# Optimization experiments

Hardware: AMD Instinct MI355X
Metric: run time of the kernel (lower is better)

Reference implementation:

```python
import jax, jax.numpy as jnp
import numpy as np
from jax import lax

F_DIM = 128
H_DIM = 128
K_NN = 16
S_PTS = 512
EPS = 1e-5


def _layernorm(x, g, b):
    m = jnp.mean(x, -1, keepdims=True)
    v = jnp.mean((x - m) ** 2, -1, keepdims=True)
    return (x - m) * lax.rsqrt(v + EPS) * g + b


def _batchnorm(x, g, b):
    # training-mode BN over (batch, points, neighbors) per channel; x: [B,S,K,C]
    m = jnp.mean(x, (0, 1, 2))
    v = jnp.mean((x - m) ** 2, (0, 1, 2))
    return (x - m) * lax.rsqrt(v + EPS) * g + b


def _gather(x, idx):
    # x: [B,R,C], idx: [B,...] int -> [B,...,C]
    return jax.vmap(lambda a, i: a[i])(x, idx)


def _fps(xyz, S):
    # farthest point sampling, deterministic start at index 0 (pytorch3d default)
    B, N, _ = xyz.shape
    idx0 = jnp.zeros((B,), jnp.int32)

    def step(carry, _):
        mind, last = carry
        p = jax.vmap(lambda a, i: a[i])(xyz, last)  # [B,3]
        d = jnp.sum((xyz - p[:, None]) ** 2, -1)  # [B,N]
        mind = jnp.minimum(mind, d)
        nxt = jnp.argmax(mind, -1).astype(jnp.int32)
        return (mind, nxt), nxt

    init = (jnp.full((B, N), 1e10, xyz.dtype), idx0)
    _, rest = lax.scan(step, init, None, length=S - 1)
    return jnp.concatenate([idx0[None], rest], 0).T  # [B,S]


def _knn_idx(q, ref, K):
    # squared dists [B,Q,R]; top-K nearest, sorted ascending by distance
    d2 = (jnp.sum(q * q, -1)[:, :, None] + jnp.sum(ref * ref, -1)[:, None, :]
          - 2.0 * jnp.einsum('bqd,brd->bqr', q, ref))
    _, idx = lax.top_k(-d2, K)
    return idx


def setup_inputs() -> dict:
    key = jax.random.key(0)
    ks = jax.random.split(key, 32)
    B, N, F, H = 4, 8192, F_DIM, H_DIM
    w = lambda k, shp: (jax.random.normal(k, shp, jnp.float32) * 0.02)
    return {
        'xyzp': jax.random.uniform(ks[0], (B, N, 4), jnp.float32),
        'features': jax.random.normal(ks[1], (B, N, F), jnp.float32),
        'ln_g': jnp.ones((F,), jnp.float32), 'ln_b': jnp.zeros((F,), jnp.float32),
        'td_w0': w(ks[2], (F + 3, F)), 'td_b0': jnp.zeros((F,), jnp.float32),
        'td_bn0_g': jnp.ones((F,), jnp.float32), 'td_bn0_b': jnp.zeros((F,), jnp.float32),
        'td_w1': w(ks[3], (F, F)), 'td_b1': jnp.zeros((F,), jnp.float32),
        'td_bn1_g': jnp.ones((F,), jnp.float32), 'td_bn1_b': jnp.zeros((F,), jnp.float32),
        'w_kern': w(ks[4], (F, H)), 'b_kern': jnp.zeros((H,), jnp.float32),
        'w_gkern': w(ks[5], (F, H)), 'b_gkern': jnp.zeros((H,), jnp.float32),
        'w_agg': w(ks[6], (H, F)), 'b_agg': jnp.zeros((F,), jnp.float32),
        'w_q': w(ks[7], (H, H)), 'w_k': w(ks[8], (H, H)), 'w_v': w(ks[9], (H, H)),
        'pe_w1': w(ks[10], (4, H)), 'pe_b1': jnp.zeros((H,), jnp.float32),
        'pe_w2': w(ks[11], (H, H)), 'pe_b2': jnp.zeros((H,), jnp.float32),
        'at_w1': w(ks[12], (H, H)), 'at_b1': jnp.zeros((H,), jnp.float32),
        'at_w2': w(ks[13], (H, H)), 'at_b2': jnp.zeros((H,), jnp.float32),
    }


def reference(xyzp, features, ln_g, ln_b, td_w0, td_b0, td_bn0_g, td_bn0_b,
              td_w1, td_b1, td_bn1_g, td_bn1_b, w_kern, b_kern, w_gkern, b_gkern,
              w_agg, b_agg, w_q, w_k, w_v, pe_w1, pe_b1, pe_w2, pe_b2,
              at_w1, at_b1, at_w2, at_b2):
    feats = _layernorm(features, ln_g, ln_b)
    xyz = xyzp[:, :, :3]
    # ---- TransitionDown ----
    fps_idx = _fps(xyz, S_PTS)                       # [B,S]
    new_xyz = _gather(xyz, fps_idx)                  # [B,S,3]
    idx_dn = _knn_idx(new_xyz, xyz, K_NN)            # [B,S,K]
    new_xyzp = _gather(xyzp, idx_dn)[:, :, 0]        # [B,S,4] nearest = self
    grouped_xyz = _gather(xyz, idx_dn) - new_xyz[:, :, None]   # [B,S,K,3]
    grouped_feat = _gather(feats, idx_dn)            # [B,S,K,F]
    h = jnp.concatenate([grouped_xyz, grouped_feat], -1)
    h = jax.nn.relu(_batchnorm(h @ td_w0 + td_b0, td_bn0_g, td_bn0_b))
    h = jax.nn.relu(_batchnorm(h @ td_w1 + td_b1, td_bn1_g, td_bn1_b))
    new_feats = jnp.max(h, axis=2)                   # [B,S,F]
    # ---- vector attention over K global neighbors ----
    idx_up = _knn_idx(xyz, new_xyz, K_NN)            # [B,N,K]
    pdiff = xyzp[:, :, None] - _gather(new_xyzp, idx_up)  # [B,N,K,4]
    pos_enc = jax.nn.relu(pdiff @ pe_w1 + pe_b1) @ pe_w2 + pe_b2
    x = feats @ w_kern + b_kern                      # [B,N,H]
    new_x = new_feats @ w_gkern + b_gkern            # [B,S,H]
    q = x @ w_q
    k = _gather(new_x @ w_k, idx_up)                 # [B,N,K,H]
    v = _gather(new_x @ w_v, idx_up)
    a = q[:, :, None] - k + pos_enc
    a = jax.nn.relu(a @ at_w1 + at_b1) @ at_w2 + at_b2
    a = jax.nn.softmax(a / np.float32(np.sqrt(H_DIM)), axis=2)  # softmax over neighbors
    res = jnp.sum(a * (v + pos_enc), axis=2)         # einsum bmnf,bmnf->bmf
    return res @ w_agg + b_agg + feats
```

## Files before the change

### kernel.cpp

```cpp
#include <hip/hip_runtime.h>

constexpr int B = 4, N = 8192, S = 512, K = 16, F = 128, H = 128;
constexpr float EPS = 1e-5f;

typedef short v8s __attribute__((ext_vector_type(8)));
typedef float v4f __attribute__((ext_vector_type(4)));

__device__ __forceinline__ short f2bf(float x) {
  union { float f; unsigned u; } v; v.f = x;
  unsigned r = v.u + 0x7fffu + ((v.u >> 16) & 1u);
  return (short)(r >> 16);
}
__device__ __forceinline__ float bf2f(short s) {
  union { unsigned u; float f; } v; v.u = ((unsigned)(unsigned short)s) << 16;
  return v.f;
}

template <int CTRL>
__device__ __forceinline__ float dpp_mov_f(float v) {
  return __int_as_float(__builtin_amdgcn_update_dpp(
      __float_as_int(v), __float_as_int(v), CTRL, 0xF, 0xF, false));
}
template <int CTRL>
__device__ __forceinline__ int dpp_mov_i(int v) {
  return __builtin_amdgcn_update_dpp(v, v, CTRL, 0xF, 0xF, false);
}

__global__ __launch_bounds__(256) void wconv_kernel(
    const float* __restrict__ pe_w2, const float* __restrict__ at_w1,
    const float* __restrict__ at_w2, const float* __restrict__ w_kern,
    const float* __restrict__ w_q, const float* __restrict__ td_w1,
    const float* __restrict__ td_w0, short* __restrict__ wbf) {
  int i = blockIdx.x * 256 + threadIdx.x;
  if (i < 6 * 16384) {
    int m = i >> 14, e = i & 16383;
    const float* src = m == 0 ? pe_w2 : m == 1 ? at_w1 : m == 2 ? at_w2
                     : m == 3 ? w_kern : m == 4 ? w_q : td_w1;
    int kx = e >> 7, n = e & 127;
    wbf[m * 16384 + n * 128 + kx] = f2bf(src[e]);
  } else {
    int e = i - 6 * 16384;
    int n = e / 160, kz = e % 160;
    short v = (kz < 131) ? f2bf(td_w0[kz * 128 + n]) : (short)0;
    wbf[6 * 16384 + n * 160 + kz] = v;
  }
}

__global__ __launch_bounds__(256) void ln_kernel(const float* __restrict__ features,
    const float* __restrict__ g, const float* __restrict__ bta, float* __restrict__ feats) {
  int r = blockIdx.x * 4 + (threadIdx.x >> 6);
  int lane = threadIdx.x & 63;
  const float2* fp = (const float2*)(features + (size_t)r * F);
  float2 v = fp[lane];
  float s = v.x + v.y;
  #pragma unroll
  for (int off = 32; off > 0; off >>= 1) s += __shfl_xor(s, off);
  float m = s * (1.f / F);
  float dx = v.x - m, dy = v.y - m;
  float s2 = dx * dx + dy * dy;
  #pragma unroll
  for (int off = 32; off > 0; off >>= 1) s2 += __shfl_xor(s2, off);
  float rstd = rsqrtf(s2 * (1.f / F) + EPS);
  float2 gg = ((const float2*)g)[lane];
  float2 bb = ((const float2*)bta)[lane];
  float2* op = (float2*)(feats + (size_t)r * F);
  op[lane] = make_float2(dx * rstd * gg.x + bb.x, dy * rstd * gg.y + bb.y);
}

__global__ __launch_bounds__(256, 1) void fps_kernel(const float* __restrict__ xyzp,
    float* __restrict__ new_xyz) {
  __shared__ float4 xl4[N];
  __shared__ float nx[S * 3];
  __shared__ float2 slot[2][4];
  int b = blockIdx.x, t = threadIdx.x;
  int lane = t & 63, wid = t >> 6;
  const float4* xp = (const float4*)(xyzp + (size_t)b * N * 4);
  float px[32], py[32], pz[32], mind[32];
  #pragma unroll
  for (int j = 0; j < 32; j++) {
    int idx = t + 256 * j;
    float4 p = xp[idx];
    px[j] = p.x; py[j] = p.y; pz[j] = p.z; mind[j] = 1e10f;
    xl4[idx] = p;
  }
  __syncthreads();
  float4 p0 = xl4[0];
  float cx = p0.x, cy = p0.y, cz = p0.z;
  if (t == 0) { nx[0] = cx; nx[1] = cy; nx[2] = cz; }
  for (int s = 1; s < S; ++s) {
    float bv = -1.f; int bj = 0;
    #pragma unroll
    for (int j = 0; j < 32; j++) {
      float dx = __fsub_rn(px[j], cx), dy = __fsub_rn(py[j], cy), dz = __fsub_rn(pz[j], cz);
      float d = __fadd_rn(__fadd_rn(__fmul_rn(dx, dx), __fmul_rn(dy, dy)), __fmul_rn(dz, dz));
      mind[j] = fminf(mind[j], d);
      if (mind[j] > bv) { bv = mind[j]; bj = j; }
    }
    int bi = t + (bj << 8);
    #define FPS_STEP(CTRL) { \
      float ov = dpp_mov_f<CTRL>(bv); int oi = dpp_mov_i<CTRL>(bi); \
      if (ov > bv || (ov == bv && oi < bi)) { bv = ov; bi = oi; } }
    FPS_STEP(0x111) FPS_STEP(0x112) FPS_STEP(0x114) FPS_STEP(0x118)
    FPS_STEP(0x142) FPS_STEP(0x143)
    #undef FPS_STEP
    int par = s & 1;
    if (lane == 63) slot[par][wid] = make_float2(bv, __int_as_float(bi));
    __syncthreads();
    float2 s0 = slot[par][0], s1 = slot[par][1], s2 = slot[par][2], s3 = slot[par][3];
    int i0 = __float_as_int(s0.y), i1 = __float_as_int(s1.y);
    int i2 = __float_as_int(s2.y), i3 = __float_as_int(s3.y);
    float4 c0v = xl4[i0], c1v = xl4[i1], c2v = xl4[i2], c3v = xl4[i3];
    float v0 = s0.x, v1 = s1.x, v2 = s2.x, v3 = s3.x;
    bool m01 = (v1 > v0) || (v1 == v0 && i1 < i0);
    float va = m01 ? v1 : v0; int ia = m01 ? i1 : i0;
    bool m23 = (v3 > v2) || (v3 == v2 && i3 < i2);
    float vb = m23 ? v3 : v2; int ib = m23 ? i3 : i2;
    bool mf = (vb > va) || (vb == va && ib < ia);
    float cax = m01 ? c1v.x : c0v.x, cay = m01 ? c1v.y : c0v.y, caz = m01 ? c1v.z : c0v.z;
    float cbx = m23 ? c3v.x : c2v.x, cby = m23 ? c3v.y : c2v.y, cbz = m23 ? c3v.z : c2v.z;
    cx = mf ? cbx : cax; cy = mf ? cby : cay; cz = mf ? cbz : caz;
    if (t == 0) { nx[s * 3 + 0] = cx; nx[s * 3 + 1] = cy; nx[s * 3 + 2] = cz; }
  }
  __syncthreads();
  for (int i = t; i < S * 3; i += 256)
    new_xyz[(size_t)b * S * 3 + i] = nx[i];
}

__global__ __launch_bounds__(256) void knn_dn_kernel(const float* __restrict__ xyzp,
    const float* __restrict__ new_xyz, int* __restrict__ idx_dn, float* __restrict__ new_xyzp) {
  int wave = threadIdx.x >> 6, lane = threadIdx.x & 63;
  int qid = blockIdx.x * 4 + wave;
  int b = qid >> 9, s = qid & (S - 1);
  const float4* xp = (const float4*)(xyzp + (size_t)b * N * 4);
  float qx = new_xyz[((size_t)b * S + s) * 3 + 0];
  float qy = new_xyz[((size_t)b * S + s) * 3 + 1];
  float qz = new_xyz[((size_t)b * S + s) * 3 + 2];
  float qq = __fadd_rn(__fadd_rn(__fmul_rn(qx, qx), __fmul_rn(qy, qy)), __fmul_rn(qz, qz));

  float lastD = -1.f; int lastI = -1;
  float D1, D2; int I1, I2;
  auto scan2 = [&]() {
    D1 = 3e38f; I1 = 0x7fffffff; D2 = 3e38f; I2 = 0x7fffffff;
    for (int j = 0; j < 128; j++) {
      int i = lane + 64 * j;
      float4 p = xp[i];
      float rr  = __fadd_rn(__fadd_rn(__fmul_rn(p.x, p.x), __fmul_rn(p.y, p.y)), __fmul_rn(p.z, p.z));
      float dot = __fadd_rn(__fadd_rn(__fmul_rn(qx, p.x), __fmul_rn(qy, p.y)), __fmul_rn(qz, p.z));
      float d2 = __fsub_rn(__fadd_rn(qq, rr), __fmul_rn(2.0f, dot));
      bool gate = (d2 > lastD) || (d2 == lastD && i > lastI);
      bool b1   = (d2 < D1) || (d2 == D1 && i < I1);
      bool b2   = (d2 < D2) || (d2 == D2 && i < I2);
      if (gate && b1)      { D2 = D1; I2 = I1; D1 = d2; I1 = i; }
      else if (gate && b2) { D2 = d2; I2 = i; }
    }
  };
  scan2();
  int outI = 0;
  float4 nn0;
  #pragma unroll 1
  for (int r = 0; r < K; r++) {
    float mD = D1; int mI = I1; int mL = lane;
    #pragma unroll
    for (int off = 32; off > 0; off >>= 1) {
      float od = __shfl_xor(mD, off); int oi = __shfl_xor(mI, off); int ol = __shfl_xor(mL, off);
      if (od < mD || (od == mD && oi < mI)) { mD = od; mI = oi; mL = ol; }
    }
    if (lane == r) outI = mI;
    if (r == 0 && lane == 0) nn0 = xp[mI];
    if (lane == mL) {
      lastD = mD; lastI = mI;
      if (I2 != 0x7fffffff) { D1 = D2; I1 = I2; D2 = 3e38f; I2 = 0x7fffffff; }
      else scan2();
    }
  }
  size_t base = ((size_t)b * S + s) * K;
  if (lane < K) idx_dn[base + lane] = outI;
  if (lane == 0) *(float4*)&new_xyzp[((size_t)b * S + s) * 4] = nn0;
}

__global__ __launch_bounds__(256) void knn_up_kernel(const float* __restrict__ xyzp,
    const float* __restrict__ new_xyz, int* __restrict__ idx_up) {
  int wave = threadIdx.x >> 6, lane = threadIdx.x & 63;
  int qid = blockIdx.x * 4 + wave;
  int b = qid >> 13, n = qid & (N - 1);
  const float4* xp = (const float4*)(xyzp + (size_t)b * N * 4);
  float4 qp = xp[n];
  float qx = qp.x, qy = qp.y, qz = qp.z;
  float qq = __fadd_rn(__fadd_rn(__fmul_rn(qx, qx), __fmul_rn(qy, qy)), __fmul_rn(qz, qz));
  float rx[8], ry[8], rz[8];
  #pragma unroll
  for (int j = 0; j < 8; j++) {
    int i = lane + 64 * j;
    rx[j] = new_xyz[((size_t)b * S + i) * 3 + 0];
    ry[j] = new_xyz[((size_t)b * S + i) * 3 + 1];
    rz[j] = new_xyz[((size_t)b * S + i) * 3 + 2];
  }
  float lastD = -1.f; int lastI = -1;
  float D1, D2; int I1, I2;
  auto scan2 = [&]() {
    D1 = 3e38f; I1 = 0x7fffffff; D2 = 3e38f; I2 = 0x7fffffff;
    #pragma unroll
    for (int j = 0; j < 8; j++) {
      int i = lane + 64 * j;
      float rr  = __fadd_rn(__fadd_rn(__fmul_rn(rx[j], rx[j]), __fmul_rn(ry[j], ry[j])), __fmul_rn(rz[j], rz[j]));
      float dot = __fadd_rn(__fadd_rn(__fmul_rn(qx, rx[j]), __fmul_rn(qy, ry[j])), __fmul_rn(qz, rz[j]));
      float d2 = __fsub_rn(__fadd_rn(qq, rr), __fmul_rn(2.0f, dot));
      bool gate = (d2 > lastD) || (d2 == lastD && i > lastI);
      bool b1   = (d2 < D1) || (d2 == D1 && i < I1);
      bool b2   = (d2 < D2) || (d2 == D2 && i < I2);
      if (gate && b1)      { D2 = D1; I2 = I1; D1 = d2; I1 = i; }
      else if (gate && b2) { D2 = d2; I2 = i; }
    }
  };
  scan2();
  int outI = 0;
  #pragma unroll 1
  for (int r = 0; r < K; r++) {
    float mD = D1; int mI = I1; int mL = lane;
    #pragma unroll
    for (int off = 32; off > 0; off >>= 1) {
      float od = __shfl_xor(mD, off); int oi = __shfl_xor(mI, off); int ol = __shfl_xor(mL, off);
      if (od < mD || (od == mD && oi < mI)) { mD = od; mI = oi; mL = ol; }
    }
    if (lane == r) outI = mI;
    if (lane == mL) {
      lastD = mD; lastI = mI;
      if (I2 != 0x7fffffff) { D1 = D2; I1 = I2; D2 = 3e38f; I2 = 0x7fffffff; }
      else scan2();
    }
  }
  size_t base = ((size_t)b * N + n) * K;
  if (lane < K) idx_up[base + lane] = outI;
}

constexpr int KS0 = 168;
__global__ __launch_bounds__(256) void td0_mfma(const float* __restrict__ xyzp,
    const float* __restrict__ new_xyz, const float* __restrict__ feats,
    const int* __restrict__ idx_dn, const short* __restrict__ w0bf, const float* __restrict__ b0,
    float* __restrict__ act0) {
  __shared__ short WT[128 * KS0];
  __shared__ short Abuf[4][16 * KS0];
  __shared__ int nbs[4][16];
  const int t = threadIdx.x, w = t >> 6, lane = t & 63;
  const int c0 = lane & 15, quad = lane >> 4;
  const int row0 = blockIdx.x * 64 + w * 16;
  const int bI = row0 >> 13;
  if (lane < 16) {
    int nb = idx_dn[row0 + lane];
    nbs[w][lane] = nb;
    int s = ((row0 + lane) >> 4) & (S - 1);
    #pragma unroll
    for (int d = 0; d < 3; d++)
      Abuf[w][lane * KS0 + d] =
          f2bf(xyzp[((size_t)bI * N + nb) * 4 + d] - new_xyz[((size_t)bI * S + s) * 3 + d]);
    for (int k2 = 131; k2 < 160; k2++) Abuf[w][lane * KS0 + k2] = 0;
  }
  #pragma unroll 4
  for (int i = 0; i < 32; i++) {
    int idx = lane + 64 * i;
    int r = idx >> 7, c = idx & 127;
    int nb = nbs[w][r];
    Abuf[w][r * KS0 + 3 + c] = f2bf(feats[((size_t)bI * N + nb) * F + c]);
  }
  #pragma unroll
  for (int i = 0; i < 10; i++) {
    int u = t + 256 * i;
    int n = u / 20, k8 = u % 20;
    *(v8s*)&WT[n * KS0 + k8 * 8] = *(const v8s*)&w0bf[n * 160 + k8 * 8];
  }
  __syncthreads();
  v4f acc[8];
  #pragma unroll
  for (int nt = 0; nt < 8; nt++) { float bvv = b0[nt * 16 + c0]; acc[nt] = (v4f){bvv, bvv, bvv, bvv}; }
  #pragma unroll
  for (int ks = 0; ks < 5; ks++) {
    v8s a = *(const v8s*)&Abuf[w][c0 * KS0 + ks * 32 + quad * 8];
    #pragma unroll
    for (int nt = 0; nt < 8; nt++) {
      v8s bf = *(const v8s*)&WT[(nt * 16 + c0) * KS0 + ks * 32 + quad * 8];
      acc[nt] = __builtin_amdgcn_mfma_f32_16x16x32_bf16(a, bf, acc[nt], 0, 0, 0);
    }
  }
  #pragma unroll
  for (int nt = 0; nt < 8; nt++)
    #pragma unroll
    for (int r = 0; r < 4; r++)
      act0[(size_t)(row0 + quad * 4 + r) * F + nt * 16 + c0] = acc[nt][r];
}

__global__ __launch_bounds__(256) void bn_reduce_kernel(const float* __restrict__ x,
                                                        float* __restrict__ sums) {
  __shared__ float ls[256], ls2[256];
  int t = threadIdx.x;
  size_t base = (size_t)blockIdx.x * 65536 + t;
  float s = 0.f, s2 = 0.f;
  for (int i = 0; i < 256; i++) {
    float v = x[base + (size_t)i * 256];
    s += v; s2 = fmaf(v, v, s2);
  }
  ls[t] = s; ls2[t] = s2; __syncthreads();
  if (t < 128) {
    s = ls[t] + ls[t + 128]; s2 = ls2[t] + ls2[t + 128];
    atomicAdd(&sums[t], s); atomicAdd(&sums[128 + t], s2);
  }
}

constexpr int KS1 = 136;
__global__ __launch_bounds__(256) void td1_mfma(const float* __restrict__ act0,
    const float* __restrict__ sums, const float* __restrict__ bn_g, const float* __restrict__ bn_b,
    const short* __restrict__ w1bf, const float* __restrict__ b1, float* __restrict__ act1) {
  __shared__ short WT[128 * KS1];
  __shared__ short Abuf[4][16 * KS1];
  __shared__ float scs[128], shs[128];
  const int t = threadIdx.x, w = t >> 6, lane = t & 63;
  const int c0 = lane & 15, quad = lane >> 4;
  const int row0 = blockIdx.x * 64 + w * 16;
  if (t < 128) {
    float m = sums[t] * (1.f / 32768.f);
    float var = sums[128 + t] * (1.f / 32768.f) - m * m;
    float rstd = rsqrtf(var + EPS);
    float sc = bn_g[t] * rstd;
    scs[t] = sc;
    shs[t] = bn_b[t] - m * sc;
  }
  #pragma unroll
  for (int i = 0; i < 8; i++) {
    int g = t + 256 * i;
    int n = g >> 4, k8 = g & 15;
    *(v8s*)&WT[n * KS1 + k8 * 8] = *(const v8s*)&w1bf[n * 128 + k8 * 8];
  }
  __syncthreads();
  #pragma unroll 4
  for (int i = 0; i < 32; i++) {
    int idx = lane + 64 * i;
    int r = idx >> 7, c = idx & 127;
    float vv = fmaxf(fmaf(act0[(size_t)(row0 + r) * F + c], scs[c], shs[c]), 0.f);
    Abuf[w][r * KS1 + c] = f2bf(vv);
  }
  v4f acc[8];
  #pragma unroll
  for (int nt = 0; nt < 8; nt++) { float bvv = b1[nt * 16 + c0]; acc[nt] = (v4f){bvv, bvv, bvv, bvv}; }
  #pragma unroll
  for (int ks = 0; ks < 4; ks++) {
    v8s a = *(const v8s*)&Abuf[w][c0 * KS1 + ks * 32 + quad * 8];
    #pragma unroll
    for (int nt = 0; nt < 8; nt++) {
      v8s bf = *(const v8s*)&WT[(nt * 16 + c0) * KS1 + ks * 32 + quad * 8];
      acc[nt] = __builtin_amdgcn_mfma_f32_16x16x32_bf16(a, bf, acc[nt], 0, 0, 0);
    }
  }
  #pragma unroll
  for (int nt = 0; nt < 8; nt++)
    #pragma unroll
    for (int r = 0; r < 4; r++)
      act1[(size_t)(row0 + quad * 4 + r) * F + nt * 16 + c0] = acc[nt][r];
}

__global__ __launch_bounds__(128) void tail_kernel(const float* __restrict__ act1,
    const float* __restrict__ sums, const float* __restrict__ bn_g, const float* __restrict__ bn_b,
    const float* __restrict__ w_gkern, const float* __restrict__ b_gkern,
    const float* __restrict__ wk, const float* __restrict__ wvp,
    float* __restrict__ kk, float* __restrict__ vv) {
  int bs = blockIdx.x, t = threadIdx.x;
  float m = sums[t] * (1.f / 32768.f);
  float var = sums[128 + t] * (1.f / 32768.f) - m * m;
  float rstd = rsqrtf(var + EPS);
  float sc = bn_g[t] * rstd;
  float sh = bn_b[t] - m * sc;
  float mx = -3e38f;
  for (int k = 0; k < K; k++) {
    float v = fmaxf(fmaf(act1[((size_t)bs * K + k) * F + t], sc, sh), 0.f);
    mx = fmaxf(mx, v);
  }
  __shared__ float row[128];
  __shared__ float row2[128];
  row[t] = mx; __syncthreads();
  {
    const float4* r4 = (const float4*)row;
    float a0 = 0.f, a1 = 0.f, a2 = 0.f, a3 = 0.f;
    #pragma unroll 8
    for (int i = 0; i < 32; i++) {
      float4 rv = r4[i];
      a0 = fmaf(rv.x, w_gkern[(4 * i + 0) * F + t], a0);
      a1 = fmaf(rv.y, w_gkern[(4 * i + 1) * F + t], a1);
      a2 = fmaf(rv.z, w_gkern[(4 * i + 2) * F + t], a2);
      a3 = fmaf(rv.w, w_gkern[(4 * i + 3) * F + t], a3);
    }
    row2[t] = b_gkern[t] + ((a0 + a1) + (a2 + a3));
  }
  __syncthreads();
  {
    const float4* r4 = (const float4*)row2;
    float k0 = 0.f, k1 = 0.f, k2 = 0.f, k3 = 0.f;
    float v0 = 0.f, v1 = 0.f, v2 = 0.f, v3 = 0.f;
    #pragma unroll 4
    for (int i = 0; i < 32; i++) {
      float4 rv = r4[i];
      k0 = fmaf(rv.x, wk[(4 * i + 0) * F + t], k0);
      k1 = fmaf(rv.y, wk[(4 * i + 1) * F + t], k1);
      k2 = fmaf(rv.z, wk[(4 * i + 2) * F + t], k2);
      k3 = fmaf(rv.w, wk[(4 * i + 3) * F + t], k3);
      v0 = fmaf(rv.x, wvp[(4 * i + 0) * F + t], v0);
      v1 = fmaf(rv.y, wvp[(4 * i + 1) * F + t], v1);
      v2 = fmaf(rv.z, wvp[(4 * i + 2) * F + t], v2);
      v3 = fmaf(rv.w, wvp[(4 * i + 3) * F + t], v3);
    }
    kk[(size_t)bs * F + t] = (k0 + k1) + (k2 + k3);
    vv[(size_t)bs * F + t] = (v0 + v1) + (v2 + v3);
  }
}

__global__ __launch_bounds__(256) void q_mfma(const float* __restrict__ feats,
    const short* __restrict__ wkbf, const float* __restrict__ b_kern,
    const short* __restrict__ wqbf, float* __restrict__ q) {
  __shared__ short WT[128 * KS1];
  __shared__ short Abuf[4][16 * KS1];
  const int t = threadIdx.x, w = t >> 6, lane = t & 63;
  const int c0 = lane & 15, quad = lane >> 4;
  const int row0 = blockIdx.x * 64 + w * 16;
  #pragma unroll 4
  for (int i = 0; i < 32; i++) {
    int idx = lane + 64 * i;
    int r = idx >> 7, c = idx & 127;
    Abuf[w][r * KS1 + c] = f2bf(feats[(size_t)(row0 + r) * F + c]);
  }
  #pragma unroll
  for (int i = 0; i < 8; i++) {
    int g = t + 256 * i;
    int n = g >> 4, k8 = g & 15;
    *(v8s*)&WT[n * KS1 + k8 * 8] = *(const v8s*)&wkbf[n * 128 + k8 * 8];
  }
  __syncthreads();
  v4f acc[8];
  #pragma unroll
  for (int nt = 0; nt < 8; nt++) { float bvv = b_kern[nt * 16 + c0]; acc[nt] = (v4f){bvv, bvv, bvv, bvv}; }
  #pragma unroll
  for (int ks = 0; ks < 4; ks++) {
    v8s a = *(const v8s*)&Abuf[w][c0 * KS1 + ks * 32 + quad * 8];
    #pragma unroll
    for (int nt = 0; nt < 8; nt++) {
      v8s bf = *(const v8s*)&WT[(nt * 16 + c0) * KS1 + ks * 32 + quad * 8];
      acc[nt] = __builtin_amdgcn_mfma_f32_16x16x32_bf16(a, bf, acc[nt], 0, 0, 0);
    }
  }
  __syncthreads();
  #pragma unroll
  for (int i = 0; i < 8; i++) {
    int g = t + 256 * i;
    int n = g >> 4, k8 = g & 15;
    *(v8s*)&WT[n * KS1 + k8 * 8] = *(const v8s*)&wqbf[n * 128 + k8 * 8];
  }
  #pragma unroll
  for (int nt = 0; nt < 8; nt++)
    #pragma unroll
    for (int r = 0; r < 4; r++)
      Abuf[w][(quad * 4 + r) * KS1 + nt * 16 + c0] = f2bf(acc[nt][r]);
  __syncthreads();
  v4f acc2[8];
  #pragma unroll
  for (int nt = 0; nt < 8; nt++) acc2[nt] = (v4f){0.f, 0.f, 0.f, 0.f};
  #pragma unroll
  for (int ks = 0; ks < 4; ks++) {
    v8s a = *(const v8s*)&Abuf[w][c0 * KS1 + ks * 32 + quad * 8];
    #pragma unroll
    for (int nt = 0; nt < 8; nt++) {
      v8s bf = *(const v8s*)&WT[(nt * 16 + c0) * KS1 + ks * 32 + quad * 8];
      acc2[nt] = __builtin_amdgcn_mfma_f32_16x16x32_bf16(a, bf, acc2[nt], 0, 0, 0);
    }
  }
  #pragma unroll
  for (int nt = 0; nt < 8; nt++)
    #pragma unroll
    for (int r = 0; r < 4; r++)
      q[(size_t)(row0 + quad * 4 + r) * F + nt * 16 + c0] = acc2[nt][r];
}

constexpr int WS = 136;
constexpr int VS = 132;

__global__ __launch_bounds__(256) void attn_kernel(const float* __restrict__ xyzp,
    const float* __restrict__ q, const float* __restrict__ kk, const float* __restrict__ vv,
    const float* __restrict__ new_xyzp, const int* __restrict__ idx_up,
    const float* __restrict__ feats, const short* __restrict__ wbf,
    const float* __restrict__ pe_w1, const float* __restrict__ pe_b1,
    const float* __restrict__ pe_b2,
    const float* __restrict__ at_b1, const float* __restrict__ at_b2,
    const float* __restrict__ w_agg, const float* __restrict__ b_agg,
    float* __restrict__ out) {
  __shared__ short WT[128 * WS];
  __shared__ short Abuf[4][16 * WS];
  __shared__ short WVb[4][16 * VS];
  __shared__ float qsh[4][128];
  __shared__ float resh[4][128];
  __shared__ float pdsh[4][16][4];
  __shared__ int   nbsh[4][16];

  const int t = threadIdx.x, w = t >> 6, lane = t & 63;
  const int c0 = lane & 15, quad = lane >> 4;
  const int p = blockIdx.x * 4 + w;
  const int b = p >> 13;

  qsh[w][lane]      = q[(size_t)p * H + lane];
  qsh[w][lane + 64] = q[(size_t)p * H + lane + 64];
  if (lane < 16) nbsh[w][lane] = idx_up[(size_t)p * K + lane];
  {
    int k = lane >> 2, d = lane & 3;
    pdsh[w][k][d] = xyzp[(size_t)p * 4 + d] - new_xyzp[((size_t)b * S + nbsh[w][k]) * 4 + d];
  }
  #pragma unroll
  for (int cc = 0; cc < 2; cc++) {
    int c = cc * 64 + lane;
    float bb = pe_b1[c];
    float w0 = pe_w1[c], w1 = pe_w1[128 + c], w2 = pe_w1[256 + c], w3 = pe_w1[384 + c];
    #pragma unroll
    for (int k = 0; k < 16; k++) {
      float h = bb + pdsh[w][k][0] * w0 + pdsh[w][k][1] * w1 + pdsh[w][k][2] * w2 + pdsh[w][k][3] * w3;
      Abuf[w][k * WS + c] = f2bf(fmaxf(h, 0.f));
    }
  }

  auto stageW = [&](const short* __restrict__ Wt) {
    __syncthreads();
    #pragma unroll
    for (int i = 0; i < 8; i++) {
      int g = t + 256 * i;
      int n = g >> 4, k8 = g & 15;
      *(v8s*)&WT[n * WS + k8 * 8] = *(const v8s*)&Wt[n * 128 + k8 * 8];
    }
    __syncthreads();
  };
  auto gemm = [&](const float* __restrict__ bias, v4f* acc) {
    #pragma unroll
    for (int nt = 0; nt < 8; nt++) {
      float bv = bias[nt * 16 + c0];
      acc[nt] = (v4f){bv, bv, bv, bv};
    }
    #pragma unroll
    for (int ks = 0; ks < 4; ks++) {
      v8s a = *(const v8s*)&Abuf[w][c0 * WS + ks * 32 + quad * 8];
      #pragma unroll
      for (int nt = 0; nt < 8; nt++) {
        v8s bf = *(const v8s*)&WT[(nt * 16 + c0) * WS + ks * 32 + quad * 8];
        acc[nt] = __builtin_amdgcn_mfma_f32_16x16x32_bf16(a, bf, acc[nt], 0, 0, 0);
      }
    }
  };

  stageW(wbf + 0 * 16384);
  v4f pe[8];
  gemm(pe_b2, pe);

  #pragma unroll
  for (int nt = 0; nt < 8; nt++) {
    #pragma unroll
    for (int r = 0; r < 4; r++) {
      int krow = quad * 4 + r;
      int c = nt * 16 + c0;
      int nb = nbsh[w][krow];
      float pev = pe[nt][r];
      float avv = qsh[w][c] - kk[((size_t)b * S + nb) * H + c] + pev;
      float wvv = vv[((size_t)b * S + nb) * H + c] + pev;
      Abuf[w][krow * WS + c] = f2bf(avv);
      WVb[w][krow * VS + c] = f2bf(wvv);
    }
  }

  stageW(wbf + 1 * 16384);
  v4f h1[8];
  gemm(at_b1, h1);
  #pragma unroll
  for (int nt = 0; nt < 8; nt++)
    #pragma unroll
    for (int r = 0; r < 4; r++)
      Abuf[w][(quad * 4 + r) * WS + nt * 16 + c0] = f2bf(fmaxf(h1[nt][r], 0.f));

  stageW(wbf + 2 * 16384);
  v4f lg[8];
  gemm(at_b2, lg);

  const float scale = 0.08838834764831845f;
  #pragma unroll
  for (int nt = 0; nt < 8; nt++) {
    float l0 = lg[nt][0] * scale, l1 = lg[nt][1] * scale;
    float l2 = lg[nt][2] * scale, l3 = lg[nt][3] * scale;
    float m = fmaxf(fmaxf(l0, l1), fmaxf(l2, l3));
    m = fmaxf(m, __shfl_xor(m, 16));
    m = fmaxf(m, __shfl_xor(m, 32));
    float e0 = expf(l0 - m), e1 = expf(l1 - m), e2 = expf(l2 - m), e3 = expf(l3 - m);
    float ssum = e0 + e1 + e2 + e3;
    ssum += __shfl_xor(ssum, 16);
    ssum += __shfl_xor(ssum, 32);
    float inv = 1.f / ssum;
    int c = nt * 16 + c0;
    float partial =
        e0 * bf2f(WVb[w][(quad * 4 + 0) * VS + c]) + e1 * bf2f(WVb[w][(quad * 4 + 1) * VS + c]) +
        e2 * bf2f(WVb[w][(quad * 4 + 2) * VS + c]) + e3 * bf2f(WVb[w][(quad * 4 + 3) * VS + c]);
    partial += __shfl_xor(partial, 16);
    partial += __shfl_xor(partial, 32);
    if (quad == 0) resh[w][c] = partial * inv;
  }
  __syncthreads();

  #pragma unroll
  for (int cc = 0; cc < 2; cc++) {
    int c = cc * 64 + lane;
    const float4* r4 = (const float4*)resh[w];
    float o0 = 0.f, o1 = 0.f, o2 = 0.f, o3 = 0.f;
    #pragma unroll 4
    for (int i = 0; i < 32; i++) {
      float4 rv = r4[i];
      o0 = fmaf(rv.x, w_agg[(4 * i + 0) * H + c], o0);
      o1 = fmaf(rv.y, w_agg[(4 * i + 1) * H + c], o1);
      o2 = fmaf(rv.z, w_agg[(4 * i + 2) * H + c], o2);
      o3 = fmaf(rv.w, w_agg[(4 * i + 3) * H + c], o3);
    }
    float o = b_agg[c] + ((o0 + o1) + (o2 + o3));
    out[(size_t)p * F + c] = o + feats[(size_t)p * F + c];
  }
}

extern "C" void kernel_launch(void* const* d_in, const int* in_sizes, int n_in,
                              void* d_out, int out_size, void* d_ws, size_t ws_size,
                              hipStream_t stream) {
  (void)in_sizes; (void)n_in; (void)out_size; (void)ws_size;
  const float* xyzp    = (const float*)d_in[0];
  const float* features= (const float*)d_in[1];
  const float* ln_g    = (const float*)d_in[2];
  const float* ln_b    = (const float*)d_in[3];
  const float* td_w0   = (const float*)d_in[4];
  const float* td_b0   = (const float*)d_in[5];
  const float* bn0_g   = (const float*)d_in[6];
  const float* bn0_b   = (const float*)d_in[7];
  const float* td_w1   = (const float*)d_in[8];
  const float* td_b1   = (const float*)d_in[9];
  const float* bn1_g   = (const float*)d_in[10];
  const float* bn1_b   = (const float*)d_in[11];
  const float* w_kern  = (const float*)d_in[12];
  const float* b_kern  = (const float*)d_in[13];
  const float* w_gkern = (const float*)d_in[14];
  const float* b_gkern = (const float*)d_in[15];
  const float* w_agg   = (const float*)d_in[16];
  const float* b_agg   = (const float*)d_in[17];
  const float* w_q     = (const float*)d_in[18];
  const float* w_k     = (const float*)d_in[19];
  const float* w_v     = (const float*)d_in[20];
  const float* pe_w1   = (const float*)d_in[21];
  const float* pe_b1   = (const float*)d_in[22];
  const float* pe_w2   = (const float*)d_in[23];
  const float* pe_b2   = (const float*)d_in[24];
  const float* at_w1   = (const float*)d_in[25];
  const float* at_b1   = (const float*)d_in[26];
  const float* at_w2   = (const float*)d_in[27];
  const float* at_b2   = (const float*)d_in[28];
  float* out = (float*)d_out;

  float* wsf = (float*)d_ws;
  float* feats     = wsf + 0;
  float* q         = wsf + 4194304;
  float* act0      = wsf + 8388608;
  float* act1      = wsf + 12582912;
  short* wbf       = (short*)(wsf + 16777216);
  float* kk        = wsf + 17301504;
  float* vv        = wsf + 17563648;
  float* new_xyz   = wsf + 17825792;
  float* new_xyzp  = wsf + 17831936;
  float* sums0     = wsf + 17840128;
  float* sums1     = wsf + 17840384;
  int* idx_dn  = (int*)(wsf + 17841152);
  int* idx_up  = idx_dn + 32768;

  hipMemsetAsync(sums0, 0, 512 * sizeof(float), stream);
  wconv_kernel<<<464, 256, 0, stream>>>(pe_w2, at_w1, at_w2, w_kern, w_q, td_w1, td_w0, wbf);
  ln_kernel<<<B * N / 4, 256, 0, stream>>>(features, ln_g, ln_b, feats);
  fps_kernel<<<B, 256, 0, stream>>>(xyzp, new_xyz);
  knn_dn_kernel<<<512, 256, 0, stream>>>(xyzp, new_xyz, idx_dn, new_xyzp);
  knn_up_kernel<<<8192, 256, 0, stream>>>(xyzp, new_xyz, idx_up);
  td0_mfma<<<512, 256, 0, stream>>>(xyzp, new_xyz, feats, idx_dn, wbf + 6 * 16384, td_b0, act0);
  bn_reduce_kernel<<<64, 256, 0, stream>>>(act0, sums0);
  td1_mfma<<<512, 256, 0, stream>>>(act0, sums0, bn0_g, bn0_b, wbf + 5 * 16384, td_b1, act1);
  bn_reduce_kernel<<<64, 256, 0, stream>>>(act1, sums1);
  tail_kernel<<<B * S, 128, 0, stream>>>(act1, sums1, bn1_g, bn1_b,
      w_gkern, b_gkern, w_k, w_v, kk, vv);
  q_mfma<<<512, 256, 0, stream>>>(feats, wbf + 3 * 16384, b_kern, wbf + 4 * 16384, q);
  attn_kernel<<<8192, 256, 0, stream>>>(xyzp, q, kk, vv, new_xyzp, idx_up, feats, wbf,
      pe_w1, pe_b1, pe_b2, at_b1, at_b2, w_agg, b_agg, out);
}
```

Measured before the change: 1.616 ms.

## Process two points per wave in attention kernel to amortize weight staging

Each wave in the attention kernel now handles two query points instead of one, and the grid is halved. Each staged weight tile in shared memory is therefore reused across twice as many GEMMs, which cuts the global-to-LDS weight traffic and the block syncs per point. The value-plus-position term is no longer stored as bf16 in LDS; it is read from global vv directly during the softmax reduction, which saves LDS space but adds scattered global loads. Register pressure goes up because both position-encoding accumulators stay live, and the lower block count may reduce occupancy.

```diff
diff --git a/kernel.cpp b/kernel.cpp
--- a/kernel.cpp
+++ b/kernel.cpp
@@ -476,7 +476,6 @@
 }
 
 constexpr int WS = 136;
-constexpr int VS = 132;
 
 __global__ __launch_bounds__(256) void attn_kernel(const float* __restrict__ xyzp,
     const float* __restrict__ q, const float* __restrict__ kk, const float* __restrict__ vv,
@@ -488,34 +487,38 @@
     const float* __restrict__ w_agg, const float* __restrict__ b_agg,
     float* __restrict__ out) {
   __shared__ short WT[128 * WS];
-  __shared__ short Abuf[4][16 * WS];
-  __shared__ short WVb[4][16 * VS];
-  __shared__ float qsh[4][128];
-  __shared__ float resh[4][128];
-  __shared__ float pdsh[4][16][4];
-  __shared__ int   nbsh[4][16];
+  __shared__ short Abuf[4][2][16 * WS];
+  __shared__ float qsh[4][2][128];
+  __shared__ float resh[4][2][128];
+  __shared__ float pdsh[4][2][16][4];
+  __shared__ int   nbsh[4][2][16];
 
   const int t = threadIdx.x, w = t >> 6, lane = t & 63;
   const int c0 = lane & 15, quad = lane >> 4;
-  const int p = blockIdx.x * 4 + w;
-  const int b = p >> 13;
-
-  qsh[w][lane]      = q[(size_t)p * H + lane];
-  qsh[w][lane + 64] = q[(size_t)p * H + lane + 64];
-  if (lane < 16) nbsh[w][lane] = idx_up[(size_t)p * K + lane];
-  {
-    int k = lane >> 2, d = lane & 3;
-    pdsh[w][k][d] = xyzp[(size_t)p * 4 + d] - new_xyzp[((size_t)b * S + nbsh[w][k]) * 4 + d];
-  }
-  #pragma unroll
-  for (int cc = 0; cc < 2; cc++) {
-    int c = cc * 64 + lane;
-    float bb = pe_b1[c];
-    float w0 = pe_w1[c], w1 = pe_w1[128 + c], w2 = pe_w1[256 + c], w3 = pe_w1[384 + c];
-    #pragma unroll
-    for (int k = 0; k < 16; k++) {
-      float h = bb + pdsh[w][k][0] * w0 + pdsh[w][k][1] * w1 + pdsh[w][k][2] * w2 + pdsh[w][k][3] * w3;
-      Abuf[w][k * WS + c] = f2bf(fmaxf(h, 0.f));
+  const int p0 = blockIdx.x * 8 + w * 2;
+  const int b = p0 >> 13;
+
+  #pragma unroll
+  for (int sub = 0; sub < 2; sub++) {
+    int p = p0 + sub;
+    qsh[w][sub][lane]      = q[(size_t)p * H + lane];
+    qsh[w][sub][lane + 64] = q[(size_t)p * H + lane + 64];
+    if (lane < 16) nbsh[w][sub][lane] = idx_up[(size_t)p * K + lane];
+    {
+      int k = lane >> 2, d = lane & 3;
+      pdsh[w][sub][k][d] = xyzp[(size_t)p * 4 + d] - new_xyzp[((size_t)b * S + nbsh[w][sub][k]) * 4 + d];
+    }
+    #pragma unroll
+    for (int cc = 0; cc < 2; cc++) {
+      int c = cc * 64 + lane;
+      float bb = pe_b1[c];
+      float w0 = pe_w1[c], w1 = pe_w1[128 + c], w2 = pe_w1[256 + c], w3 = pe_w1[384 + c];
+      #pragma unroll
+      for (int k = 0; k < 16; k++) {
+        float h = bb + pdsh[w][sub][k][0] * w0 + pdsh[w][sub][k][1] * w1 +
+                  pdsh[w][sub][k][2] * w2 + pdsh[w][sub][k][3] * w3;
+        Abuf[w][sub][k * WS + c] = f2bf(fmaxf(h, 0.f));
+      }
     }
   }
 
@@ -529,7 +532,7 @@
     }
     __syncthreads();
   };
-  auto gemm = [&](const float* __restrict__ bias, v4f* acc) {
+  auto gemm = [&](int sub, const float* __restrict__ bias, v4f* acc) {
     #pragma unroll
     for (int nt = 0; nt < 8; nt++) {
       float bv = bias[nt * 16 + c0];
@@ -537,7 +540,7 @@
     }
     #pragma unroll
     for (int ks = 0; ks < 4; ks++) {
-      v8s a = *(const v8s*)&Abuf[w][c0 * WS + ks * 32 + quad * 8];
+      v8s a = *(const v8s*)&Abuf[w][sub][c0 * WS + ks * 32 + quad * 8];
       #pragma unroll
       for (int nt = 0; nt < 8; nt++) {
         v8s bf = *(const v8s*)&WT[(nt * 16 + c0) * WS + ks * 32 + quad * 8];
@@ -547,75 +550,91 @@
   };
 
   stageW(wbf + 0 * 16384);
-  v4f pe[8];
-  gemm(pe_b2, pe);
-
-  #pragma unroll
-  for (int nt = 0; nt < 8; nt++) {
-    #pragma unroll
-    for (int r = 0; r < 4; r++) {
-      int krow = quad * 4 + r;
+  v4f peA[8], peB[8];
+  gemm(0, pe_b2, peA);
+  gemm(1, pe_b2, peB);
+
+  #pragma unroll
+  for (int sub = 0; sub < 2; sub++) {
+    v4f* pe = sub ? peB : peA;
+    #pragma unroll
+    for (int nt = 0; nt < 8; nt++) {
+      #pragma unroll
+      for (int r = 0; r < 4; r++) {
+        int krow = quad * 4 + r;
+        int c = nt * 16 + c0;
+        int nb = nbsh[w][sub][krow];
+        float avv = qsh[w][sub][c] - kk[((size_t)b * S + nb) * H + c] + pe[nt][r];
+        Abuf[w][sub][krow * WS + c] = f2bf(avv);
+      }
+    }
+  }
+
+  stageW(wbf + 1 * 16384);
+  {
+    v4f h1[8];
+    gemm(0, at_b1, h1);
+    #pragma unroll
+    for (int nt = 0; nt < 8; nt++)
+      #pragma unroll
+      for (int r = 0; r < 4; r++)
+        Abuf[w][0][(quad * 4 + r) * WS + nt * 16 + c0] = f2bf(fmaxf(h1[nt][r], 0.f));
+    gemm(1, at_b1, h1);
+    #pragma unroll
+    for (int nt = 0; nt < 8; nt++)
+      #pragma unroll
+      for (int r = 0; r < 4; r++)
+        Abuf[w][1][(quad * 4 + r) * WS + nt * 16 + c0] = f2bf(fmaxf(h1[nt][r], 0.f));
+  }
+
+  stageW(wbf + 2 * 16384);
+  const float scale = 0.08838834764831845f;
+  #pragma unroll
+  for (int sub = 0; sub < 2; sub++) {
+    v4f lg[8];
+    gemm(sub, at_b2, lg);
+    v4f* pe = sub ? peB : peA;
+    int p = p0 + sub;
+    #pragma unroll
+    for (int nt = 0; nt < 8; nt++) {
+      float l0 = lg[nt][0] * scale, l1 = lg[nt][1] * scale;
+      float l2 = lg[nt][2] * scale, l3 = lg[nt][3] * scale;
+      float m = fmaxf(fmaxf(l0, l1), fmaxf(l2, l3));
+      m = fmaxf(m, __shfl_xor(m, 16));
+      m = fmaxf(m, __shfl_xor(m, 32));
+      float e0 = expf(l0 - m), e1 = expf(l1 - m), e2 = expf(l2 - m), e3 = expf(l3 - m);
+      float ssum = e0 + e1 + e2 + e3;
+      ssum += __shfl_xor(ssum, 16);
+      ssum += __shfl_xor(ssum, 32);
+      float inv = 1.f / ssum;
       int c = nt * 16 + c0;
-      int nb = nbsh[w][krow];
-      float pev = pe[nt][r];
-      float avv = qsh[w][c] - kk[((size_t)b * S + nb) * H + c] + pev;
-      float wvv = vv[((size_t)b * S + nb) * H + c] + pev;
-      Abuf[w][krow * WS + c] = f2bf(avv);
-      WVb[w][krow * VS + c] = f2bf(wvv);
-    }
-  }
-
-  stageW(wbf + 1 * 16384);
-  v4f h1[8];
-  gemm(at_b1, h1);
-  #pragma unroll
-  for (int nt = 0; nt < 8; nt++)
-    #pragma unroll
-    for (int r = 0; r < 4; r++)
-      Abuf[w][(quad * 4 + r) * WS + nt * 16 + c0] = f2bf(fmaxf(h1[nt][r], 0.f));
-
-  stageW(wbf + 2 * 16384);
-  v4f lg[8];
-  gemm(at_b2, lg);
-
-  const float scale = 0.08838834764831845f;
-  #pragma unroll
-  for (int nt = 0; nt < 8; nt++) {
-    float l0 = lg[nt][0] * scale, l1 = lg[nt][1] * scale;
-    float l2 = lg[nt][2] * scale, l3 = lg[nt][3] * scale;
-    float m = fmaxf(fmaxf(l0, l1), fmaxf(l2, l3));
-    m = fmaxf(m, __shfl_xor(m, 16));
-    m = fmaxf(m, __shfl_xor(m, 32));
-    float e0 = expf(l0 - m), e1 = expf(l1 - m), e2 = expf(l2 - m), e3 = expf(l3 - m);
-    float ssum = e0 + e1 + e2 + e3;
-    ssum += __shfl_xor(ssum, 16);
-    ssum += __shfl_xor(ssum, 32);
-    float inv = 1.f / ssum;
-    int c = nt * 16 + c0;
-    float partial =
-        e0 * bf2f(WVb[w][(quad * 4 + 0) * VS + c]) + e1 * bf2f(WVb[w][(quad * 4 + 1) * VS + c]) +
-        e2 * bf2f(WVb[w][(quad * 4 + 2) * VS + c]) + e3 * bf2f(WVb[w][(quad * 4 + 3) * VS + c]);
-    partial += __shfl_xor(partial, 16);
-    partial += __shfl_xor(partial, 32);
-    if (quad == 0) resh[w][c] = partial * inv;
-  }
-  __syncthreads();
-
-  #pragma unroll
-  for (int cc = 0; cc < 2; cc++) {
-    int c = cc * 64 + lane;
-    const float4* r4 = (const float4*)resh[w];
-    float o0 = 0.f, o1 = 0.f, o2 = 0.f, o3 = 0.f;
-    #pragma unroll 4
-    for (int i = 0; i < 32; i++) {
-      float4 rv = r4[i];
-      o0 = fmaf(rv.x, w_agg[(4 * i + 0) * H + c], o0);
-      o1 = fmaf(rv.y, w_agg[(4 * i + 1) * H + c], o1);
-      o2 = fmaf(rv.z, w_agg[(4 * i + 2) * H + c], o2);
-      o3 = fmaf(rv.w, w_agg[(4 * i + 3) * H + c], o3);
-    }
-    float o = b_agg[c] + ((o0 + o1) + (o2 + o3));
-    out[(size_t)p * F + c] = o + feats[(size_t)p * F + c];
+      int nb0 = nbsh[w][sub][quad * 4 + 0], nb1 = nbsh[w][sub][quad * 4 + 1];
+      int nb2 = nbsh[w][sub][quad * 4 + 2], nb3 = nbsh[w][sub][quad * 4 + 3];
+      float partial =
+          e0 * (vv[((size_t)b * S + nb0) * H + c] + pe[nt][0]) +
+          e1 * (vv[((size_t)b * S + nb1) * H + c] + pe[nt][1]) +
+          e2 * (vv[((size_t)b * S + nb2) * H + c] + pe[nt][2]) +
+          e3 * (vv[((size_t)b * S + nb3) * H + c] + pe[nt][3]);
+      partial += __shfl_xor(partial, 16);
+      partial += __shfl_xor(partial, 32);
+      if (quad == 0) resh[w][sub][c] = partial * inv;
+    }
+    #pragma unroll
+    for (int cc = 0; cc < 2; cc++) {
+      int c = cc * 64 + lane;
+      const float4* r4 = (const float4*)resh[w][sub];
+      float o0 = 0.f, o1 = 0.f, o2 = 0.f, o3 = 0.f;
+      #pragma unroll 4
+      for (int i = 0; i < 32; i++) {
+        float4 rv = r4[i];
+        o0 = fmaf(rv.x, w_agg[(4 * i + 0) * H + c], o0);
+        o1 = fmaf(rv.y, w_agg[(4 * i + 1) * H + c], o1);
+        o2 = fmaf(rv.z, w_agg[(4 * i + 2) * H + c], o2);
+        o3 = fmaf(rv.w, w_agg[(4 * i + 3) * H + c], o3);
+      }
+      float o = b_agg[c] + ((o0 + o1) + (o2 + o3));
+      out[(size_t)p * F + c] = o + feats[(size_t)p * F + c];
+    }
   }
 }
 
@@ -682,6 +701,6 @@
   tail_kernel<<<B * S, 128, 0, stream>>>(act1, sums1, bn1_g, bn1_b,
       w_gkern, b_gkern, w_k, w_v, kk, vv);
   q_mfma<<<512, 256, 0, stream>>>(feats, wbf + 3 * 16384, b_kern, wbf + 4 * 16384, q);
-  attn_kernel<<<8192, 256, 0, stream>>>(xyzp, q, kk, vv, new_xyzp, idx_up, feats, wbf,
+  attn_kernel<<<4096, 256, 0, stream>>>(xyzp, q, kk, vv, new_xyzp, idx_up, feats, wbf,
       pe_w1, pe_b1, pe_b2, at_b1, at_b2, w_agg, b_agg, out);
 }
```

Measured after the change: 1.704 ms. 1.05x slower.
